# Kernel optimization log

Measured on AMD Instinct MI355X. Metric: run time of the kernel, lower is better.

Reference implementation:

```python
import jax, jax.numpy as jnp
import numpy as np

N, E, DIN, DOUT = 10000, 640000, 128, 256
BN_EPS = 1e-5
GIN_EPS = 0.0  # GINConv default eps, train_eps=False


def setup_inputs() -> dict:
    key = jax.random.key(0)
    ks = jax.random.split(key, 10)
    x = jax.random.normal(ks[0], (N, DIN), dtype=jnp.float32)
    edge_index = jax.random.randint(ks[1], (2, E), 0, N, dtype=jnp.int64)
    s1 = 1.0 / np.sqrt(DIN)
    s2 = 1.0 / np.sqrt(DOUT)
    return {
        "x": x,
        "edge_index": edge_index,
        "W1": jax.random.uniform(ks[2], (DIN, DOUT), jnp.float32, -s1, s1),
        "b1": jax.random.uniform(ks[3], (DOUT,), jnp.float32, -s1, s1),
        "gamma1": jnp.ones((DOUT,), jnp.float32),
        "beta1": jnp.zeros((DOUT,), jnp.float32),
        "W2": jax.random.uniform(ks[4], (DOUT, DOUT), jnp.float32, -s2, s2),
        "b2": jax.random.uniform(ks[5], (DOUT,), jnp.float32, -s2, s2),
        "gamma2": jnp.ones((DOUT,), jnp.float32),
        "beta2": jnp.zeros((DOUT,), jnp.float32),
    }


def _batchnorm(h, gamma, beta):
    # training-mode BatchNorm1d: batch statistics, biased variance
    mean = jnp.mean(h, axis=0)
    var = jnp.mean(jnp.square(h - mean), axis=0)
    return gamma * (h - mean) * jax.lax.rsqrt(var + BN_EPS) + beta


def reference(x, edge_index, W1, b1, gamma1, beta1, W2, b2, gamma2, beta2):
    src, dst = edge_index[0], edge_index[1]
    # GINConv: out_i = MLP((1+eps)*x_i + sum_{j->i} x_j)
    agg = jax.ops.segment_sum(x[src], dst, num_segments=N)  # [N, DIN]
    h = (1.0 + GIN_EPS) * x + agg
    # MLP: Linear -> BN -> ReLU -> Linear
    h = h @ W1 + b1
    h = jax.nn.relu(_batchnorm(h, gamma1, beta1))
    h = h @ W2 + b2
    # outer BN + ReLU
    return jax.nn.relu(_batchnorm(h, gamma2, beta2))
```

## Files before the change

kernel.cpp:

```cpp
#include <hip/hip_runtime.h>

#define NN 10000
#define DIN 128
#define DOUT 256
#define NB 128
#define PAD 192
#define NTILES (NN / 16)
static constexpr float BN_EPS = 1e-5f;

using short8 = __attribute__((ext_vector_type(8))) short;
using f32x4  = __attribute__((ext_vector_type(4))) float;

__device__ __forceinline__ unsigned short bf16r(float f) {
    unsigned int u = __float_as_uint(f);
    u += 0x7FFFu + ((u >> 16) & 1u);
    return (unsigned short)(u >> 16);
}
__device__ __forceinline__ float bf16f(unsigned short h) {
    return __uint_as_float((unsigned int)h << 16);
}
__device__ __forceinline__ int fragidx(int k, int n) {
    return ((k >> 5) << 13) | ((n >> 4) << 9) |
           ((((k >> 3) & 3) << 4 | (n & 15)) << 3) | (k & 7);
}

__global__ __launch_bounds__(256) void khist_prep(
    const int* __restrict__ ei, int* __restrict__ hist_g, int E,
    const float* __restrict__ x, ushort* __restrict__ xb,
    const float* __restrict__ W1, ushort* __restrict__ w1f,
    const float* __restrict__ W2, ushort* __restrict__ w2f,
    float* __restrict__ stats) {
    const int tid = threadIdx.x;
    if (blockIdx.x < NB) {
        __shared__ int hist[NN];
        for (int i = tid; i < NN; i += 256) hist[i] = 0;
        __syncthreads();
        const int chunk = (E + NB - 1) / NB;
        const int e0 = blockIdx.x * chunk;
        const int e1 = min(e0 + chunk, E);
        for (int e = e0 + tid; e < e1; e += 256) {
            atomicAdd(&hist[ei[E + e]], 1);
        }
        __syncthreads();
        int* dst = hist_g + (size_t)blockIdx.x * NN;
        for (int i = tid; i < NN; i += 256) dst[i] = hist[i];
    } else {
        const int pt = (blockIdx.x - NB) * 256 + tid;
        if (pt < 8192) stats[pt] = 0.f;
        for (int i = pt; i < NN * DIN / 4; i += 32768) {
            const float4 v = reinterpret_cast<const float4*>(x)[i];
            ushort4 o;
            o.x = bf16r(v.x); o.y = bf16r(v.y);
            o.z = bf16r(v.z); o.w = bf16r(v.w);
            reinterpret_cast<ushort4*>(xb)[i] = o;
        }
        {
            const int k = pt >> 8, n = pt & 255;
            w1f[fragidx(k, n)] = bf16r(W1[pt]);
        }
        for (int i = pt; i < 256 * 256; i += 32768) {
            const int k = i >> 8, n = i & 255;
            w2f[fragidx(k, n)] = bf16r(W2[i]);
        }
    }
}

__global__ __launch_bounds__(256) void kscan_a(int* __restrict__ hist_g,
                                               int* __restrict__ total) {
    const int node = blockIdx.x * 256 + threadIdx.x;
    if (node >= NN) return;
    int run = 0;
#pragma unroll 8
    for (int b = 0; b < NB; ++b) {
        const int v = hist_g[(size_t)b * NN + node];
        hist_g[(size_t)b * NN + node] = run;
        run += v;
    }
    total[node] = run;
}

__global__ __launch_bounds__(256) void kfill(const int* __restrict__ ei,
                                             const int* __restrict__ hist_g,
                                             int* __restrict__ edge_src,
                                             int E) {
    __shared__ int cur[NN];
    const int tid = threadIdx.x;
    const int* base = hist_g + (size_t)blockIdx.x * NN;
    for (int i = tid; i < NN; i += 256) cur[i] = i * PAD + base[i];
    __syncthreads();
    const int chunk = (E + NB - 1) / NB;
    const int e0 = blockIdx.x * chunk;
    const int e1 = min(e0 + chunk, E);
    for (int e = e0 + tid; e < e1; e += 256) {
        const int src = ei[e];
        const int dst = ei[E + e];
        const int pos = atomicAdd(&cur[dst], 1);
        edge_src[pos] = src;
    }
}

__global__ __launch_bounds__(256) void gemm1_k(
    const float* __restrict__ x, const ushort* __restrict__ xb,
    const int* __restrict__ total, const int* __restrict__ edge_src,
    const ushort* __restrict__ w1f, const float* __restrict__ b1,
    ushort* __restrict__ h1f, float* __restrict__ sum1,
    float* __restrict__ sq1) {
    __shared__ short a_lds[4 * 64 * 8];
    __shared__ float work[6208];
    short* b_lds = (short*)work;
    float* hrow  = work;
    float* red_s = work + 4160;
    float* red_q = work + 5184;
    const int tid = threadIdx.x;
    const int w = tid >> 6, l = tid & 63;
    const int m = blockIdx.x;
    const int hw = tid >> 5, c4 = tid & 31;
    const ushort4* xb4 = reinterpret_cast<const ushort4*>(xb);

#pragma unroll
    for (int r = 0; r < 2; ++r) {
        const int row = r * 8 + hw;
        const int node = m * 16 + row;
        const int beg = node * PAD;
        const int end = beg + total[node];

        float4 a0 = make_float4(0.f, 0.f, 0.f, 0.f);
        float4 a1 = a0, a2 = a0, a3 = a0;
        int j = beg;
        for (; j + 7 < end; j += 8) {
            int s[8];
#pragma unroll
            for (int t = 0; t < 8; ++t) s[t] = edge_src[j + t];
            ushort4 v[8];
#pragma unroll
            for (int t = 0; t < 8; ++t) v[t] = xb4[(size_t)s[t] * 32 + c4];
#pragma unroll
            for (int t = 0; t < 8; ++t) {
                float4* a = (t & 3) == 0 ? &a0 : (t & 3) == 1 ? &a1
                          : (t & 3) == 2 ? &a2 : &a3;
                a->x += bf16f(v[t].x);
                a->y += bf16f(v[t].y);
                a->z += bf16f(v[t].z);
                a->w += bf16f(v[t].w);
            }
        }
        for (; j < end; ++j) {
            const ushort4 v = xb4[(size_t)edge_src[j] * 32 + c4];
            a0.x += bf16f(v.x); a0.y += bf16f(v.y);
            a0.z += bf16f(v.z); a0.w += bf16f(v.w);
        }
        const float4 xv =
            reinterpret_cast<const float4*>(x)[(size_t)node * 32 + c4];
        ushort4 o;
        o.x = bf16r(xv.x + a0.x + a1.x + a2.x + a3.x);
        o.y = bf16r(xv.y + a0.y + a1.y + a2.y + a3.y);
        o.z = bf16r(xv.z + a0.z + a1.z + a2.z + a3.z);
        o.w = bf16r(xv.w + a0.w + a1.w + a2.w + a3.w);
        const int c = c4 >> 3, kg = (c4 >> 1) & 3, half = c4 & 1;
        *reinterpret_cast<ushort4*>(
            (char*)a_lds + c * 1024 + ((kg << 4) + row) * 16 + half * 8) = o;
    }

    f32x4 acc[4];
#pragma unroll
    for (int p = 0; p < 4; ++p) {
        const float b = b1[(w * 4 + p) * 16 + (l & 15)];
        acc[p] = (f32x4){b, b, b, b};
    }

    for (int c = 0; c < 4; ++c) {
        __syncthreads();
        const float4* src = ((const float4*)w1f) + c * 1024;
#pragma unroll
        for (int i = 0; i < 4; ++i)
            ((float4*)b_lds)[tid + 256 * i] = src[tid + 256 * i];
        __syncthreads();
        const short8 a = ((const short8*)a_lds)[c * 64 + l];
#pragma unroll
        for (int p = 0; p < 4; ++p) {
            const short8 b = ((const short8*)b_lds)[(w * 4 + p) * 64 + l];
            acc[p] = __builtin_amdgcn_mfma_f32_16x16x32_bf16(a, b, acc[p],
                                                             0, 0, 0);
        }
    }
    __syncthreads();

#pragma unroll
    for (int p = 0; p < 4; ++p) {
        const int col = (w * 4 + p) * 16 + (l & 15);
        float s = 0.f, q = 0.f;
#pragma unroll
        for (int r = 0; r < 4; ++r) {
            const float v = acc[p][r];
            hrow[((l >> 4) * 4 + r) * 260 + col] = v;
            s += v;
            q += v * v;
        }
        red_s[(l >> 4) * 256 + col] = s;
        red_q[(l >> 4) * 256 + col] = q;
    }
    __syncthreads();
    {
        float s = 0.f, q = 0.f;
#pragma unroll
        for (int g = 0; g < 4; ++g) {
            s += red_s[g * 256 + tid];
            q += red_q[g * 256 + tid];
        }
        atomicAdd(&sum1[(m & 7) * 256 + tid], s);
        atomicAdd(&sq1[(m & 7) * 256 + tid], q);
    }
#pragma unroll
    for (int t = 0; t < 2; ++t) {
        const int u = tid + t * 256;
        const int c2 = u >> 6, kg = (u >> 4) & 3, row = u & 15;
        const float* src = &hrow[row * 260 + c2 * 32 + kg * 8];
        short8 g;
#pragma unroll
        for (int jj = 0; jj < 8; ++jj) g[jj] = (short)bf16r(src[jj]);
        ((short8*)h1f)[m * 512 + u] = g;
    }
}

__global__ __launch_bounds__(256) void gemm2_k(
    const ushort* __restrict__ h1f, const float* __restrict__ sum1,
    const float* __restrict__ sq1, const float* __restrict__ gamma1,
    const float* __restrict__ beta1, const ushort* __restrict__ w2f,
    const float* __restrict__ b2, float* __restrict__ h2,
    float* __restrict__ sum2, float* __restrict__ sq2) {
    __shared__ short a_lds[8 * 64 * 8];
    __shared__ float work[6208];
    __shared__ float sc1[DOUT], sh1[DOUT];
    short* b_lds = (short*)work;
    float* hrow  = work;
    float* red_s = work + 4160;
    float* red_q = work + 5184;
    const int tid = threadIdx.x;
    const int w = tid >> 6, l = tid & 63;
    const int m = blockIdx.x;

    {
        float s = 0.f, q = 0.f;
#pragma unroll
        for (int i = 0; i < 8; ++i) {
            s += sum1[i * 256 + tid];
            q += sq1[i * 256 + tid];
        }
        const float nInv = 1.0f / (float)NN;
        const float mean = s * nInv;
        const float var = q * nInv - mean * mean;
        const float sc = gamma1[tid] * rsqrtf(var + BN_EPS);
        sc1[tid] = sc;
        sh1[tid] = beta1[tid] - mean * sc;
    }
    __syncthreads();

#pragma unroll
    for (int t = 0; t < 2; ++t) {
        const int u = tid + 256 * t;
        const int col0 = ((u >> 6) << 5) + (((u >> 4) & 3) << 3);
        const short8 hv = ((const short8*)h1f)[m * 512 + u];
        short8 g;
#pragma unroll
        for (int jj = 0; jj < 8; ++jj) {
            const float f = bf16f((unsigned short)hv[jj]);
            const float r = fmaxf(fmaf(f, sc1[col0 + jj], sh1[col0 + jj]), 0.f);
            g[jj] = (short)bf16r(r);
        }
        ((short8*)a_lds)[u] = g;
    }

    f32x4 acc[4];
#pragma unroll
    for (int p = 0; p < 4; ++p) {
        const float b = b2[(w * 4 + p) * 16 + (l & 15)];
        acc[p] = (f32x4){b, b, b, b};
    }

    for (int c = 0; c < 8; ++c) {
        __syncthreads();
        const float4* src = ((const float4*)w2f) + c * 1024;
#pragma unroll
        for (int i = 0; i < 4; ++i)
            ((float4*)b_lds)[tid + 256 * i] = src[tid + 256 * i];
        __syncthreads();
        const short8 a = ((const short8*)a_lds)[c * 64 + l];
#pragma unroll
        for (int p = 0; p < 4; ++p) {
            const short8 b = ((const short8*)b_lds)[(w * 4 + p) * 64 + l];
            acc[p] = __builtin_amdgcn_mfma_f32_16x16x32_bf16(a, b, acc[p],
                                                             0, 0, 0);
        }
    }
    __syncthreads();

#pragma unroll
    for (int p = 0; p < 4; ++p) {
        const int col = (w * 4 + p) * 16 + (l & 15);
        float s = 0.f, q = 0.f;
#pragma unroll
        for (int r = 0; r < 4; ++r) {
            const float v = acc[p][r];
            hrow[((l >> 4) * 4 + r) * 260 + col] = v;
            s += v;
            q += v * v;
        }
        red_s[(l >> 4) * 256 + col] = s;
        red_q[(l >> 4) * 256 + col] = q;
    }
    __syncthreads();
    {
        float s = 0.f, q = 0.f;
#pragma unroll
        for (int g = 0; g < 4; ++g) {
            s += red_s[g * 256 + tid];
            q += red_q[g * 256 + tid];
        }
        atomicAdd(&sum2[(m & 7) * 256 + tid], s);
        atomicAdd(&sq2[(m & 7) * 256 + tid], q);
    }
#pragma unroll
    for (int i = 0; i < 4; ++i) {
        const int idx = tid + 256 * i;
        const int row = idx >> 6, col4 = idx & 63;
        const float4 v = *(const float4*)&hrow[row * 260 + col4 * 4];
        ((float4*)h2)[(size_t)(m * 16 + row) * 64 + col4] = v;
    }
}

__global__ __launch_bounds__(256) void bn_relu_out_k(
    const float* __restrict__ h2, const float* __restrict__ sum2,
    const float* __restrict__ sq2, const float* __restrict__ gamma2,
    const float* __restrict__ beta2, float* __restrict__ out) {
    __shared__ float sc2[DOUT], sh2[DOUT];
    const int tid = threadIdx.x;
    {
        float s = 0.f, q = 0.f;
#pragma unroll
        for (int i = 0; i < 8; ++i) {
            s += sum2[i * 256 + tid];
            q += sq2[i * 256 + tid];
        }
        const float nInv = 1.0f / (float)NN;
        const float mean = s * nInv;
        const float var = q * nInv - mean * mean;
        const float sc = gamma2[tid] * rsqrtf(var + BN_EPS);
        sc2[tid] = sc;
        sh2[tid] = beta2[tid] - mean * sc;
    }
    __syncthreads();
#pragma unroll
    for (int i = 0; i < 4; ++i) {
        const int u = blockIdx.x * 1024 + i * 256 + tid;
        const int k4 = u & 63;
        const float4 h = reinterpret_cast<const float4*>(h2)[u];
        const float4 sc = reinterpret_cast<const float4*>(sc2)[k4];
        const float4 sh = reinterpret_cast<const float4*>(sh2)[k4];
        float4 g;
        g.x = fmaxf(fmaf(h.x, sc.x, sh.x), 0.f);
        g.y = fmaxf(fmaf(h.y, sc.y, sh.y), 0.f);
        g.z = fmaxf(fmaf(h.z, sc.z, sh.z), 0.f);
        g.w = fmaxf(fmaf(h.w, sc.w, sh.w), 0.f);
        reinterpret_cast<float4*>(out)[u] = g;
    }
}

extern "C" void kernel_launch(void* const* d_in, const int* in_sizes, int n_in,
                              void* d_out, int out_size, void* d_ws,
                              size_t ws_size, hipStream_t stream) {
    const float* x      = (const float*)d_in[0];
    const int*   ei     = (const int*)d_in[1];
    const float* W1     = (const float*)d_in[2];
    const float* b1     = (const float*)d_in[3];
    const float* gamma1 = (const float*)d_in[4];
    const float* beta1  = (const float*)d_in[5];
    const float* W2     = (const float*)d_in[6];
    const float* b2     = (const float*)d_in[7];
    const float* gamma2 = (const float*)d_in[8];
    const float* beta2  = (const float*)d_in[9];
    const int E = in_sizes[1] / 2;

    char* w = (char*)d_ws;
    size_t off = 0;
    float* stats = (float*)(w + off); off += 32768;
    float* sum1 = stats + 0;
    float* sq1  = stats + 2048;
    float* sum2 = stats + 4096;
    float* sq2  = stats + 6144;
    int* hist_g   = (int*)(w + off); off += (size_t)NB * NN * 4;
    int* total    = (int*)(w + off); off += 40064;
    int* edge_src = (int*)(w + off); off += (size_t)NN * PAD * 4;
    ushort* xb    = (ushort*)(w + off); off += (size_t)NN * DIN * 2;
    ushort* w1f   = (ushort*)(w + off); off += 65536;
    ushort* w2f   = (ushort*)(w + off); off += 131072;
    ushort* h1f   = (ushort*)(w + off); off += (size_t)NN * DOUT * 2;
    float* h2     = (float*)(w + off); off += (size_t)NN * DOUT * 4;
    float* out    = (float*)d_out;

    khist_prep<<<2 * NB, 256, 0, stream>>>(ei, hist_g, E, x, xb, W1, w1f,
                                           W2, w2f, stats);
    kscan_a<<<40, 256, 0, stream>>>(hist_g, total);
    kfill<<<NB, 256, 0, stream>>>(ei, hist_g, edge_src, E);
    gemm1_k<<<NTILES, 256, 0, stream>>>(x, xb, total, edge_src, w1f, b1,
                                        h1f, sum1, sq1);
    gemm2_k<<<NTILES, 256, 0, stream>>>(h1f, sum1, sq1, gamma1, beta1, w2f,
                                        b2, h2, sum2, sq2);
    bn_relu_out_k<<<NN * DOUT / 4 / 1024, 256, 0, stream>>>(h2, sum2, sq2,
                                                            gamma2, beta2, out);
}
```

Measured before the change: 83.26 us.

## Record per-edge rank during histogram to make CSR fill atomic-free

The histogram pass now stores, for each edge, the value returned by its shared-memory atomic increment, and the per-block histograms are kept as 16-bit values instead of 32-bit. The fill kernel then computes each edge's slot directly from the scanned block offset plus this stored rank, so it no longer needs to initialize a 10000-entry LDS cursor array or perform atomics, and it runs on a larger grid-stride launch. This halves the hist_g traffic in the scan and removes the LDS setup, at the cost of writing and rereading an extra E-sized 16-bit rank array. The 16-bit narrowing relies on per-block and per-node counts fitting in 16 bits.

```diff
diff --git a/kernel.cpp b/kernel.cpp
--- a/kernel.cpp
+++ b/kernel.cpp
@@ -25,7 +25,8 @@
 }
 
 __global__ __launch_bounds__(256) void khist_prep(
-    const int* __restrict__ ei, int* __restrict__ hist_g, int E,
+    const int* __restrict__ ei, ushort* __restrict__ hist_g,
+    ushort* __restrict__ rank, int E,
     const float* __restrict__ x, ushort* __restrict__ xb,
     const float* __restrict__ W1, ushort* __restrict__ w1f,
     const float* __restrict__ W2, ushort* __restrict__ w2f,
@@ -39,11 +40,11 @@
         const int e0 = blockIdx.x * chunk;
         const int e1 = min(e0 + chunk, E);
         for (int e = e0 + tid; e < e1; e += 256) {
-            atomicAdd(&hist[ei[E + e]], 1);
-        }
-        __syncthreads();
-        int* dst = hist_g + (size_t)blockIdx.x * NN;
-        for (int i = tid; i < NN; i += 256) dst[i] = hist[i];
+            rank[e] = (ushort)atomicAdd(&hist[ei[E + e]], 1);
+        }
+        __syncthreads();
+        ushort* dst = hist_g + (size_t)blockIdx.x * NN;
+        for (int i = tid; i < NN; i += 256) dst[i] = (ushort)hist[i];
     } else {
         const int pt = (blockIdx.x - NB) * 256 + tid;
         if (pt < 8192) stats[pt] = 0.f;
@@ -65,7 +66,7 @@
     }
 }
 
-__global__ __launch_bounds__(256) void kscan_a(int* __restrict__ hist_g,
+__global__ __launch_bounds__(256) void kscan_a(ushort* __restrict__ hist_g,
                                                int* __restrict__ total) {
     const int node = blockIdx.x * 256 + threadIdx.x;
     if (node >= NN) return;
@@ -73,28 +74,25 @@
 #pragma unroll 8
     for (int b = 0; b < NB; ++b) {
         const int v = hist_g[(size_t)b * NN + node];
-        hist_g[(size_t)b * NN + node] = run;
+        hist_g[(size_t)b * NN + node] = (ushort)run;
         run += v;
     }
     total[node] = run;
 }
 
 __global__ __launch_bounds__(256) void kfill(const int* __restrict__ ei,
-                                             const int* __restrict__ hist_g,
+                                             const ushort* __restrict__ hist_g,
+                                             const ushort* __restrict__ rank,
                                              int* __restrict__ edge_src,
                                              int E) {
-    __shared__ int cur[NN];
-    const int tid = threadIdx.x;
-    const int* base = hist_g + (size_t)blockIdx.x * NN;
-    for (int i = tid; i < NN; i += 256) cur[i] = i * PAD + base[i];
-    __syncthreads();
     const int chunk = (E + NB - 1) / NB;
-    const int e0 = blockIdx.x * chunk;
-    const int e1 = min(e0 + chunk, E);
-    for (int e = e0 + tid; e < e1; e += 256) {
+    for (int e = blockIdx.x * 256 + threadIdx.x; e < E;
+         e += gridDim.x * 256) {
         const int src = ei[e];
         const int dst = ei[E + e];
-        const int pos = atomicAdd(&cur[dst], 1);
+        const int b = e / chunk;
+        const int pos = dst * PAD + (int)hist_g[(size_t)b * NN + dst]
+                        + (int)rank[e];
         edge_src[pos] = src;
     }
 }
@@ -387,7 +385,8 @@
     float* sq1  = stats + 2048;
     float* sum2 = stats + 4096;
     float* sq2  = stats + 6144;
-    int* hist_g   = (int*)(w + off); off += (size_t)NB * NN * 4;
+    ushort* hist_g = (ushort*)(w + off); off += (size_t)NB * NN * 2;
+    ushort* rank   = (ushort*)(w + off); off += (size_t)E * 2;
     int* total    = (int*)(w + off); off += 40064;
     int* edge_src = (int*)(w + off); off += (size_t)NN * PAD * 4;
     ushort* xb    = (ushort*)(w + off); off += (size_t)NN * DIN * 2;
@@ -397,10 +396,10 @@
     float* h2     = (float*)(w + off); off += (size_t)NN * DOUT * 4;
     float* out    = (float*)d_out;
 
-    khist_prep<<<2 * NB, 256, 0, stream>>>(ei, hist_g, E, x, xb, W1, w1f,
-                                           W2, w2f, stats);
+    khist_prep<<<2 * NB, 256, 0, stream>>>(ei, hist_g, rank, E, x, xb,
+                                           W1, w1f, W2, w2f, stats);
     kscan_a<<<40, 256, 0, stream>>>(hist_g, total);
-    kfill<<<NB, 256, 0, stream>>>(ei, hist_g, edge_src, E);
+    kfill<<<256, 256, 0, stream>>>(ei, hist_g, rank, edge_src, E);
     gemm1_k<<<NTILES, 256, 0, stream>>>(x, xb, total, edge_src, w1f, b1,
                                         h1f, sum1, sq1);
     gemm2_k<<<NTILES, 256, 0, stream>>>(h1f, sum1, sq1, gamma1, beta1, w2f,
```

Measured after the change: 79.35 us. 1.05x faster.
